# Kernel tuning notes

Measured on AMD Instinct MI355X. Metric: run time of the kernel, lower is better.

The kernel has to match this reference:

```python
import jax, jax.numpy as jnp
import numpy as np

N, E, B = 100000, 800000, 32
TEXT, H, R, L = 768, 128, 8, 2
D, P, RANK = 16, 16, 8
SCALING = 16.0 / RANK  # LoRA alpha / rank


def setup_inputs() -> dict:
    key = jax.random.key(0)
    k = jax.random.split(key, 24)
    g = lambda i, shape, s=0.02: jax.random.normal(k[i], shape, dtype=jnp.float32) * s
    z = lambda shape: jnp.zeros(shape, jnp.float32)
    prop = g(7, (P, H), 0.02).at[0].set(0.0)  # property_emb row 0 zeroed (torch init)
    return {
        "x_text": jax.random.normal(k[0], (N, TEXT), jnp.float32),
        "x_path": jax.random.normal(k[1], (N, TEXT), jnp.float32),
        "text_proj_w": g(2, (TEXT, H)), "text_proj_b": z((H,)),
        "path_proj_w": g(3, (TEXT, H)), "path_proj_b": z((H,)),
        "domain_emb": g(4, (D, H), 1.0),
        "property_emb": prop,
        "path_fusion_w": g(5, (H, H)), "path_fusion_b": z((H,)),
        "pgate1_w": g(6, (2 * H, H)), "pgate1_b": z((H,)),
        "pgate2_w": g(8, (H, H)), "pgate2_b": z((H,)),
        "sem_w": g(9, (H, H)), "sem_b": z((H,)),
        "str_w": g(10, (H, H)), "str_b": z((H,)),
        "gate1_w": g(11, (2 * H, H)), "gate1_b": z((H,)),
        "gate2_w": g(12, (H, H)), "gate2_b": z((H,)),
        "rgcn_rel_w": g(13, (L, R, H, H)),
        "rgcn_root_w": g(14, (L, H, H)),
        "rgcn_bias": z((L, H)),
        "lora_a": g(15, (L, H, RANK)),
        "lora_b": g(16, (L, RANK, H)),
        "edge_index": jax.random.randint(k[17], (2, E), 0, N),
        "edge_type": jax.random.randint(k[18], (E,), 0, R),
        "batch": jnp.sort(jax.random.randint(k[19], (N,), 0, B)),
        "domain_ids": jax.random.randint(k[20], (B,), 0, D),
        "edge_property_id": jax.random.randint(k[21], (E,), 0, P),
    }


def reference(x_text, x_path, text_proj_w, text_proj_b, path_proj_w, path_proj_b,
              domain_emb, property_emb, path_fusion_w, path_fusion_b,
              pgate1_w, pgate1_b, pgate2_w, pgate2_b,
              sem_w, sem_b, str_w, str_b, gate1_w, gate1_b, gate2_w, gate2_b,
              rgcn_rel_w, rgcn_root_w, rgcn_bias, lora_a, lora_b,
              edge_index, edge_type, batch, domain_ids, edge_property_id):
    n = x_text.shape[0]
    num_layers, num_rel = rgcn_rel_w.shape[0], rgcn_rel_w.shape[1]
    src, dst = edge_index[0], edge_index[1]

    # text/path projections modulated by per-graph domain embedding
    h = x_text @ text_proj_w + text_proj_b                     # [N, H]
    d_nodes = domain_emb[domain_ids][batch]                    # [N, H]
    h = h * d_nodes
    path_ctx = (x_path @ path_proj_w + path_proj_b) * d_nodes
    path_ctx = path_ctx @ path_fusion_w + path_fusion_b
    pg = jax.nn.sigmoid(
        jax.nn.relu(jnp.concatenate([h, path_ctx], -1) @ pgate1_w + pgate1_b)
        @ pgate2_w + pgate2_b)
    h = pg * h + (1.0 - pg) * path_ctx

    # edge-property scatter-mean keyed by edge source node
    prop_ids = jnp.clip(edge_property_id, 0, property_emb.shape[0] - 1)
    pe = property_emb[prop_ids]                                # [E, H]
    ones_e = jnp.ones(src.shape, h.dtype)
    deg = jnp.maximum(jax.ops.segment_sum(ones_e, src, num_segments=n), 1.0)
    prop_agg = jax.ops.segment_sum(pe, src, num_segments=n) / deg[:, None]
    h = h + prop_agg                                           # _apply_property_prompts

    # RGCN: per-(dst, relation) mean aggregation, counts precomputed once
    seg = dst * num_rel + edge_type                            # composite segment id
    cnt = jax.ops.segment_sum(ones_e, seg, num_segments=n * num_rel)
    cnt = jnp.maximum(cnt, 1.0).reshape(n, num_rel, 1)

    curr = h
    for l in range(num_layers):
        curr_in = curr + prop_agg                              # _edge_property_message add
        sums = jax.ops.segment_sum(curr_in[src], seg, num_segments=n * num_rel)
        agg = sums.reshape(n, num_rel, -1) / cnt               # [N, R, H]
        conv = (jnp.einsum('nrh,rhd->nd', agg, rgcn_rel_w[l])
                + curr_in @ rgcn_root_w[l] + rgcn_bias[l])
        lora = (curr_in @ lora_a[l]) @ lora_b[l] * SCALING
        curr = jax.nn.relu(conv + lora)

    # semantic/structural gated fusion
    sem = h @ sem_w + sem_b
    stru = curr @ str_w + str_b
    fg = jax.nn.sigmoid(
        jax.nn.relu(jnp.concatenate([sem, stru], -1) @ gate1_w + gate1_b)
        @ gate2_w + gate2_b)
    return fg * sem + (1.0 - fg) * stru
```

## Files before the change

### kernel.cpp

```cpp
#include <hip/hip_runtime.h>
#include <cstdint>
#include <cstddef>

#define HDIM 128
#define GBM 64
#define GBK 32

__device__ __forceinline__ float sigmoidf_(float x) {
  return 1.0f / (1.0f + __expf(-x));
}

__global__ __launch_bounds__(256) void gemm128_f32(
    const float* __restrict__ A, const float* __restrict__ Wg,
    const float* __restrict__ bias, float* __restrict__ C,
    int M, int K, int accumulate, int post,
    long long strideWz, long long strideCz)
{
  __shared__ float As[GBM][GBK + 1];
  __shared__ float Ws[GBK][HDIM + 4];
  const float* Wp = Wg + (long long)blockIdx.z * strideWz;
  float* Cp = C + (long long)blockIdx.z * strideCz;
  const int m0 = blockIdx.x * GBM;
  const int tid = threadIdx.x;
  const int tx = tid & 15;
  const int ty = tid >> 4;

  float acc[4][8];
#pragma unroll
  for (int i = 0; i < 4; ++i)
#pragma unroll
    for (int j = 0; j < 8; ++j) acc[i][j] = 0.f;

  const int lar = tid >> 2;
  const int lac = (tid & 3) * 8;
  const int lwk = tid >> 3;
  const int lwj = (tid & 7) * 16;

  for (int k0 = 0; k0 < K; k0 += GBK) {
    float4 v0 = make_float4(0.f, 0.f, 0.f, 0.f), v1 = v0;
    {
      int gr = m0 + lar;
      if (gr < M) {
        const float* src = A + (long long)gr * K + (k0 + lac);
        v0 = *(const float4*)(src);
        v1 = *(const float4*)(src + 4);
      }
    }
    const float* wsrc = Wp + (long long)(k0 + lwk) * HDIM + lwj;
    float4 w0 = *(const float4*)(wsrc);
    float4 w1 = *(const float4*)(wsrc + 4);
    float4 w2 = *(const float4*)(wsrc + 8);
    float4 w3 = *(const float4*)(wsrc + 12);

    As[lar][lac + 0] = v0.x; As[lar][lac + 1] = v0.y;
    As[lar][lac + 2] = v0.z; As[lar][lac + 3] = v0.w;
    As[lar][lac + 4] = v1.x; As[lar][lac + 5] = v1.y;
    As[lar][lac + 6] = v1.z; As[lar][lac + 7] = v1.w;
    {
      float* wd = &Ws[lwk][lwj];
      wd[0]  = w0.x; wd[1]  = w0.y; wd[2]  = w0.z; wd[3]  = w0.w;
      wd[4]  = w1.x; wd[5]  = w1.y; wd[6]  = w1.z; wd[7]  = w1.w;
      wd[8]  = w2.x; wd[9]  = w2.y; wd[10] = w2.z; wd[11] = w2.w;
      wd[12] = w3.x; wd[13] = w3.y; wd[14] = w3.z; wd[15] = w3.w;
    }
    __syncthreads();

#pragma unroll 8
    for (int kk = 0; kk < GBK; ++kk) {
      float a0 = As[ty * 4 + 0][kk];
      float a1 = As[ty * 4 + 1][kk];
      float a2 = As[ty * 4 + 2][kk];
      float a3 = As[ty * 4 + 3][kk];
      float4 wa = *(const float4*)&Ws[kk][tx * 8];
      float4 wb = *(const float4*)&Ws[kk][tx * 8 + 4];
      float w[8] = {wa.x, wa.y, wa.z, wa.w, wb.x, wb.y, wb.z, wb.w};
#pragma unroll
      for (int j = 0; j < 8; ++j) {
        acc[0][j] += a0 * w[j];
        acc[1][j] += a1 * w[j];
        acc[2][j] += a2 * w[j];
        acc[3][j] += a3 * w[j];
      }
    }
    __syncthreads();
  }

#pragma unroll
  for (int i = 0; i < 4; ++i) {
    int gr = m0 + ty * 4 + i;
    if (gr >= M) continue;
    float* crow = Cp + (long long)gr * HDIM + tx * 8;
    float v[8];
#pragma unroll
    for (int j = 0; j < 8; ++j) v[j] = acc[i][j];
    if (bias) {
#pragma unroll
      for (int j = 0; j < 8; ++j) v[j] += bias[tx * 8 + j];
    }
    if (accumulate) {
      float4 c0 = *(const float4*)crow;
      float4 c1 = *(const float4*)(crow + 4);
      v[0] += c0.x; v[1] += c0.y; v[2] += c0.z; v[3] += c0.w;
      v[4] += c1.x; v[5] += c1.y; v[6] += c1.z; v[7] += c1.w;
    }
    if (post == 1) {
#pragma unroll
      for (int j = 0; j < 8; ++j) v[j] = fmaxf(v[j], 0.f);
    }
    *(float4*)crow = make_float4(v[0], v[1], v[2], v[3]);
    *(float4*)(crow + 4) = make_float4(v[4], v[5], v[6], v[7]);
  }
}

__global__ __launch_bounds__(256) void k_dnode(
    float* __restrict__ h, float* __restrict__ pc,
    const int* __restrict__ batch, const int* __restrict__ dom_ids,
    const float* __restrict__ dom_emb, int ntot)
{
  int idx = blockIdx.x * 256 + threadIdx.x;
  if (idx >= ntot) return;
  int n = idx >> 7, j = idx & 127;
  float d = dom_emb[dom_ids[batch[n]] * HDIM + j];
  h[idx] *= d;
  pc[idx] *= d;
}

__global__ __launch_bounds__(256) void k_combine(
    float* __restrict__ h, const float* __restrict__ pc,
    const float* __restrict__ pglin, const float* __restrict__ pa, int ntot)
{
  int idx = blockIdx.x * 256 + threadIdx.x;
  if (idx >= ntot) return;
  float pg = sigmoidf_(pglin[idx]);
  h[idx] = pg * h[idx] + (1.f - pg) * pc[idx] + pa[idx];
}

__global__ __launch_bounds__(256) void k_add(
    const float* __restrict__ a, const float* __restrict__ b,
    float* __restrict__ c, int ntot)
{
  int idx = blockIdx.x * 256 + threadIdx.x;
  if (idx >= ntot) return;
  c[idx] = a[idx] + b[idx];
}

__global__ __launch_bounds__(256) void k_out(
    const float* __restrict__ fglin, const float* __restrict__ sem,
    const float* __restrict__ stru, float* __restrict__ out, int ntot)
{
  int idx = blockIdx.x * 256 + threadIdx.x;
  if (idx >= ntot) return;
  float fg = sigmoidf_(fglin[idx]);
  out[idx] = fg * sem[idx] + (1.f - fg) * stru[idx];
}

__global__ __launch_bounds__(256) void k_edgecount(
    const int* __restrict__ ei, const int* __restrict__ etype,
    const int* __restrict__ epid, int* __restrict__ cntp,
    int* __restrict__ cnt8, int E)
{
  int e = blockIdx.x * 256 + threadIdx.x;
  if (e >= E) return;
  int s = ei[e];
  int d = ei[E + e];
  int et = etype[e];
  int p = epid[e];
  p = p < 0 ? 0 : (p > 15 ? 15 : p);
  atomicAdd(&cntp[s * 16 + p], 1);
  atomicAdd(&cnt8[d * 8 + et], 1);
}

__global__ __launch_bounds__(256) void k_propagg(
    const int* __restrict__ cntp, const float* __restrict__ pemb,
    float* __restrict__ pa, int ntot)
{
  int idx = blockIdx.x * 256 + threadIdx.x;
  if (idx >= ntot) return;
  int n = idx >> 7, j = idx & 127;
  int deg = 0;
  float acc = 0.f;
#pragma unroll
  for (int p = 0; p < 16; ++p) {
    int c = cntp[n * 16 + p];
    deg += c;
    acc += (float)c * pemb[p * HDIM + j];
  }
  pa[idx] = acc / (float)(deg > 1 ? deg : 1);
}

__global__ __launch_bounds__(256) void k_invcnt(
    const int* __restrict__ cnt8, float* __restrict__ invc, int ntot)
{
  int idx = blockIdx.x * 256 + threadIdx.x;
  if (idx >= ntot) return;
  int c = cnt8[idx];
  invc[idx] = 1.f / (float)(c > 1 ? c : 1);
}

__global__ __launch_bounds__(256) void k_scatter(
    const int* __restrict__ ei, const int* __restrict__ etype,
    const float* __restrict__ invc, const float* __restrict__ Y,
    float* __restrict__ conv, int E, int NN, int r0, int rc)
{
  int t = blockIdx.x * 256 + threadIdx.x;
  int e = t >> 7;
  int j = t & 127;
  if (e >= E) return;
  int et = etype[e];
  if (et < r0 || et >= r0 + rc) return;
  int s = ei[e];
  int d = ei[E + e];
  float w = invc[d * 8 + et];
  float v = Y[((long long)(et - r0) * NN + s) * HDIM + j] * w;
  atomicAdd(&conv[(long long)d * HDIM + j], v);
}

__global__ __launch_bounds__(256) void k_lora_relu(
    const float* __restrict__ xin, const float* __restrict__ conv,
    const float* __restrict__ la, const float* __restrict__ lb,
    float* __restrict__ outc, int NN)
{
  __shared__ float xs[16][129];
  __shared__ float las[128 * 8];
  __shared__ float lbs[8 * 128];
  __shared__ float Tsh[16][9];
  int tid = threadIdx.x;
  int n0 = blockIdx.x * 16;

  for (int i = tid; i < 1024; i += 256) {
    las[i] = la[i];
    lbs[i] = lb[i];
  }
  for (int i = tid; i < 16 * 128; i += 256) {
    int nn = i >> 7, j = i & 127;
    int g = n0 + nn;
    xs[nn][j] = (g < NN) ? xin[(long long)g * HDIM + j] : 0.f;
  }
  __syncthreads();

  if (tid < 128) {
    int nn = tid >> 3, r = tid & 7;
    float s = 0.f;
#pragma unroll 16
    for (int k = 0; k < 128; ++k) s += xs[nn][k] * las[k * 8 + r];
    Tsh[nn][r] = s;
  }
  __syncthreads();

  int nn = tid >> 4;
  int j0 = (tid & 15) * 8;
  int g = n0 + nn;
  if (g < NN) {
    const float* cv = conv + (long long)g * HDIM + j0;
    float* op = outc + (long long)g * HDIM + j0;
    float o[8];
#pragma unroll
    for (int jj = 0; jj < 8; ++jj) {
      float s = 0.f;
#pragma unroll
      for (int r = 0; r < 8; ++r) s += Tsh[nn][r] * lbs[r * HDIM + j0 + jj];
      float v = cv[jj] + 2.0f * s;
      o[jj] = fmaxf(v, 0.f);
    }
    *(float4*)op = make_float4(o[0], o[1], o[2], o[3]);
    *(float4*)(op + 4) = make_float4(o[4], o[5], o[6], o[7]);
  }
}

extern "C" void kernel_launch(void* const* d_in, const int* in_sizes, int n_in,
                              void* d_out, int out_size, void* d_ws, size_t ws_size,
                              hipStream_t stream)
{
  const int N = 100000, E = 800000, TEXT = 768, H = 128, R = 8, L = 2;
  const int NTOT = N * H;

  const float* x_text  = (const float*)d_in[0];
  const float* x_path  = (const float*)d_in[1];
  const float* text_w  = (const float*)d_in[2];
  const float* text_b  = (const float*)d_in[3];
  const float* path_w  = (const float*)d_in[4];
  const float* path_b  = (const float*)d_in[5];
  const float* dom_emb = (const float*)d_in[6];
  const float* prop_emb= (const float*)d_in[7];
  const float* pf_w    = (const float*)d_in[8];
  const float* pf_b    = (const float*)d_in[9];
  const float* pg1_w   = (const float*)d_in[10];
  const float* pg1_b   = (const float*)d_in[11];
  const float* pg2_w   = (const float*)d_in[12];
  const float* pg2_b   = (const float*)d_in[13];
  const float* sem_w   = (const float*)d_in[14];
  const float* sem_b   = (const float*)d_in[15];
  const float* str_w   = (const float*)d_in[16];
  const float* str_b   = (const float*)d_in[17];
  const float* g1_w    = (const float*)d_in[18];
  const float* g1_b    = (const float*)d_in[19];
  const float* g2_w    = (const float*)d_in[20];
  const float* g2_b    = (const float*)d_in[21];
  const float* rel_w   = (const float*)d_in[22];
  const float* root_w  = (const float*)d_in[23];
  const float* rbias   = (const float*)d_in[24];
  const float* lora_a  = (const float*)d_in[25];
  const float* lora_b  = (const float*)d_in[26];
  const int*   ei      = (const int*)d_in[27];
  const int*   etype   = (const int*)d_in[28];
  const int*   batch   = (const int*)d_in[29];
  const int*   dom_ids = (const int*)d_in[30];
  const int*   epid    = (const int*)d_in[31];
  float* out = (float*)d_out;

  const size_t NB = (size_t)NTOT * sizeof(float);
  char* p = (char*)d_ws;
  auto alloc = [&](size_t bytes) -> void* {
    char* q = p;
    p += (bytes + 255) & ~(size_t)255;
    return (void*)q;
  };
  float* hbuf  = (float*)alloc(NB);
  float* pabuf = (float*)alloc(NB);
  float* curr  = (float*)alloc(NB);
  float* cin   = (float*)alloc(NB);
  float* conv  = (float*)alloc(NB);
  float* tmp   = (float*)alloc(NB);
  int*   cntp  = (int*)alloc((size_t)N * 16 * 4);
  int*   cnt8  = (int*)alloc((size_t)N * 8 * 4);
  float* invc  = (float*)alloc((size_t)N * 8 * 4);
  size_t used = (size_t)(p - (char*)d_ws);

  float* ybuf = tmp;
  int RC = 1;
  if (ws_size > used) {
    size_t k = (ws_size - used) / NB;
    if (k >= 1) {
      RC = (int)(k < 8 ? k : 8);
      ybuf = (float*)alloc(NB * (size_t)RC);
    }
  }

  const int GM = (N + GBM - 1) / GBM;
  const int EWG = (NTOT + 255) / 256;

  auto gemm = [&](const float* A, const float* W, const float* b, float* C,
                  int K, int accv, int post, int zc,
                  long long swz, long long scz) {
    gemm128_f32<<<dim3(GM, 1, zc), dim3(256), 0, stream>>>(
        A, W, b, C, N, K, accv, post, swz, scz);
  };

  hipMemsetAsync(cntp, 0, (size_t)N * 24 * 4, stream);
  k_edgecount<<<(E + 255) / 256, 256, 0, stream>>>(ei, etype, epid, cntp, cnt8, E);
  k_propagg<<<EWG, 256, 0, stream>>>(cntp, prop_emb, pabuf, NTOT);
  k_invcnt<<<(N * 8 + 255) / 256, 256, 0, stream>>>(cnt8, invc, N * 8);

  gemm(x_text, text_w, text_b, hbuf, TEXT, 0, 0, 1, 0, 0);
  gemm(x_path, path_w, path_b, curr, TEXT, 0, 0, 1, 0, 0);
  k_dnode<<<EWG, 256, 0, stream>>>(hbuf, curr, batch, dom_ids, dom_emb, NTOT);
  gemm(curr, pf_w, pf_b, cin, H, 0, 0, 1, 0, 0);
  gemm(hbuf, pg1_w, pg1_b, conv, H, 0, 0, 1, 0, 0);
  gemm(cin, pg1_w + H * H, nullptr, conv, H, 1, 1, 1, 0, 0);
  gemm(conv, pg2_w, pg2_b, tmp, H, 0, 0, 1, 0, 0);
  k_combine<<<EWG, 256, 0, stream>>>(hbuf, cin, tmp, pabuf, NTOT);

  for (int l = 0; l < L; ++l) {
    const float* src = (l == 0) ? hbuf : curr;
    k_add<<<EWG, 256, 0, stream>>>(src, pabuf, cin, NTOT);
    gemm(cin, root_w + (size_t)l * H * H, rbias + (size_t)l * H,
         conv, H, 0, 0, 1, 0, 0);
    for (int r0 = 0; r0 < R; r0 += RC) {
      int rc = (R - r0) < RC ? (R - r0) : RC;
      gemm(cin, rel_w + ((size_t)l * R + r0) * H * H, nullptr, ybuf,
           H, 0, 0, rc, (long long)H * H, (long long)NTOT);
      k_scatter<<<(E * 128 + 255) / 256, 256, 0, stream>>>(
          ei, etype, invc, ybuf, conv, E, N, r0, rc);
    }
    k_lora_relu<<<(N + 15) / 16, 256, 0, stream>>>(
        cin, conv, lora_a + (size_t)l * H * 8, lora_b + (size_t)l * 8 * H,
        curr, N);
  }

  gemm(hbuf, sem_w, sem_b, conv, H, 0, 0, 1, 0, 0);
  gemm(curr, str_w, str_b, cin, H, 0, 0, 1, 0, 0);
  gemm(conv, g1_w, g1_b, tmp, H, 0, 0, 1, 0, 0);
  gemm(cin, g1_w + H * H, nullptr, tmp, H, 1, 1, 1, 0, 0);
  gemm(tmp, g2_w, g2_b, pabuf, H, 0, 0, 1, 0, 0);
  k_out<<<EWG, 256, 0, stream>>>(pabuf, conv, cin, out, NTOT);
}
```

Before: 3.732 ms.

## Replace per-relation transform-and-scatter with CSR gather aggregation then one fused GEMM

Builds a per-(dst, relation) CSR index once, using a prefix scan over the edge counts and an atomic fill of source ids. Each RGCN layer now gathers and mean-aggregates neighbour features into an [N, R*H] buffer, then does one K=1024 GEMM against the stacked relation weights. This removes the eight per-relation GEMMs and the float atomic scatter over E×128 elements. The shared GEMM kernel is also retiled to 128-row blocks with an 8x8 per-thread micro-tile and a transposed A tile. The cost is a large aggregation buffer whose size no longer checks the available workspace.

```diff
diff --git a/kernel.cpp b/kernel.cpp
--- a/kernel.cpp
+++ b/kernel.cpp
@@ -3,112 +3,112 @@
 #include <cstddef>
 
 #define HDIM 128
-#define GBM 64
-#define GBK 32
+#define TM 128
+#define TK 32
+#define SCHUNK 1024
 
 __device__ __forceinline__ float sigmoidf_(float x) {
   return 1.0f / (1.0f + __expf(-x));
 }
 
-__global__ __launch_bounds__(256) void gemm128_f32(
-    const float* __restrict__ A, const float* __restrict__ Wg,
+__global__ __launch_bounds__(256) void gemm128(
+    const float* __restrict__ A, const float* __restrict__ W,
     const float* __restrict__ bias, float* __restrict__ C,
-    int M, int K, int accumulate, int post,
-    long long strideWz, long long strideCz)
-{
-  __shared__ float As[GBM][GBK + 1];
-  __shared__ float Ws[GBK][HDIM + 4];
-  const float* Wp = Wg + (long long)blockIdx.z * strideWz;
-  float* Cp = C + (long long)blockIdx.z * strideCz;
-  const int m0 = blockIdx.x * GBM;
+    int M, int K, int accumulate, int post)
+{
+  __shared__ float At[TK][TM + 4];
+  __shared__ float Ws[TK][HDIM + 4];
+  const int m0 = blockIdx.x * TM;
   const int tid = threadIdx.x;
   const int tx = tid & 15;
   const int ty = tid >> 4;
 
-  float acc[4][8];
-#pragma unroll
-  for (int i = 0; i < 4; ++i)
+  float acc[8][8];
+#pragma unroll
+  for (int i = 0; i < 8; ++i)
 #pragma unroll
     for (int j = 0; j < 8; ++j) acc[i][j] = 0.f;
 
-  const int lar = tid >> 2;
-  const int lac = (tid & 3) * 8;
-  const int lwk = tid >> 3;
-  const int lwj = (tid & 7) * 16;
-
-  for (int k0 = 0; k0 < K; k0 += GBK) {
-    float4 v0 = make_float4(0.f, 0.f, 0.f, 0.f), v1 = v0;
-    {
-      int gr = m0 + lar;
-      if (gr < M) {
-        const float* src = A + (long long)gr * K + (k0 + lac);
-        v0 = *(const float4*)(src);
-        v1 = *(const float4*)(src + 4);
+  const int arow = tid >> 3;
+  const int ac4  = (tid & 7) * 4;
+  const int wrow = tid >> 5;
+  const int wc4  = (tid & 31) * 4;
+
+  for (int k0 = 0; k0 < K; k0 += TK) {
+#pragma unroll
+    for (int q = 0; q < 4; ++q) {
+      int row = q * 32 + arow;
+      int gr = m0 + row;
+      float4 v = make_float4(0.f, 0.f, 0.f, 0.f);
+      if (gr < M) v = *(const float4*)(A + (long long)gr * K + k0 + ac4);
+      At[ac4 + 0][row] = v.x;
+      At[ac4 + 1][row] = v.y;
+      At[ac4 + 2][row] = v.z;
+      At[ac4 + 3][row] = v.w;
+    }
+#pragma unroll
+    for (int q = 0; q < 4; ++q) {
+      int row = q * 8 + wrow;
+      float4 v = *(const float4*)(W + (long long)(k0 + row) * HDIM + wc4);
+      *(float4*)&Ws[row][wc4] = v;
+    }
+    __syncthreads();
+
+#pragma unroll 8
+    for (int kk = 0; kk < TK; ++kk) {
+      float4 a0 = *(const float4*)&At[kk][ty * 4];
+      float4 a1 = *(const float4*)&At[kk][64 + ty * 4];
+      float4 w0 = *(const float4*)&Ws[kk][tx * 4];
+      float4 w1 = *(const float4*)&Ws[kk][64 + tx * 4];
+      float a[8] = {a0.x, a0.y, a0.z, a0.w, a1.x, a1.y, a1.z, a1.w};
+      float w[8] = {w0.x, w0.y, w0.z, w0.w, w1.x, w1.y, w1.z, w1.w};
+#pragma unroll
+      for (int i = 0; i < 8; ++i)
+#pragma unroll
+        for (int j = 0; j < 8; ++j)
+          acc[i][j] += a[i] * w[j];
+    }
+    __syncthreads();
+  }
+
+  float bv[8];
+  if (bias) {
+#pragma unroll
+    for (int j = 0; j < 4; ++j) {
+      bv[j]     = bias[tx * 4 + j];
+      bv[4 + j] = bias[64 + tx * 4 + j];
+    }
+  } else {
+#pragma unroll
+    for (int j = 0; j < 8; ++j) bv[j] = 0.f;
+  }
+#pragma unroll
+  for (int i = 0; i < 8; ++i) {
+    int row = (i < 4) ? (ty * 4 + i) : (64 + ty * 4 + i - 4);
+    int gr = m0 + row;
+    if (gr >= M) continue;
+    float* cp = C + (long long)gr * HDIM;
+    float v0[4], v1[4];
+#pragma unroll
+    for (int j = 0; j < 4; ++j) {
+      v0[j] = acc[i][j] + bv[j];
+      v1[j] = acc[i][4 + j] + bv[4 + j];
+    }
+    if (accumulate) {
+      float4 c0 = *(const float4*)(cp + tx * 4);
+      float4 c1 = *(const float4*)(cp + 64 + tx * 4);
+      v0[0] += c0.x; v0[1] += c0.y; v0[2] += c0.z; v0[3] += c0.w;
+      v1[0] += c1.x; v1[1] += c1.y; v1[2] += c1.z; v1[3] += c1.w;
+    }
+    if (post == 1) {
+#pragma unroll
+      for (int j = 0; j < 4; ++j) {
+        v0[j] = fmaxf(v0[j], 0.f);
+        v1[j] = fmaxf(v1[j], 0.f);
       }
     }
-    const float* wsrc = Wp + (long long)(k0 + lwk) * HDIM + lwj;
-    float4 w0 = *(const float4*)(wsrc);
-    float4 w1 = *(const float4*)(wsrc + 4);
-    float4 w2 = *(const float4*)(wsrc + 8);
-    float4 w3 = *(const float4*)(wsrc + 12);
-
-    As[lar][lac + 0] = v0.x; As[lar][lac + 1] = v0.y;
-    As[lar][lac + 2] = v0.z; As[lar][lac + 3] = v0.w;
-    As[lar][lac + 4] = v1.x; As[lar][lac + 5] = v1.y;
-    As[lar][lac + 6] = v1.z; As[lar][lac + 7] = v1.w;
-    {
-      float* wd = &Ws[lwk][lwj];
-      wd[0]  = w0.x; wd[1]  = w0.y; wd[2]  = w0.z; wd[3]  = w0.w;
-      wd[4]  = w1.x; wd[5]  = w1.y; wd[6]  = w1.z; wd[7]  = w1.w;
-      wd[8]  = w2.x; wd[9]  = w2.y; wd[10] = w2.z; wd[11] = w2.w;
-      wd[12] = w3.x; wd[13] = w3.y; wd[14] = w3.z; wd[15] = w3.w;
-    }
-    __syncthreads();
-
-#pragma unroll 8
-    for (int kk = 0; kk < GBK; ++kk) {
-      float a0 = As[ty * 4 + 0][kk];
-      float a1 = As[ty * 4 + 1][kk];
-      float a2 = As[ty * 4 + 2][kk];
-      float a3 = As[ty * 4 + 3][kk];
-      float4 wa = *(const float4*)&Ws[kk][tx * 8];
-      float4 wb = *(const float4*)&Ws[kk][tx * 8 + 4];
-      float w[8] = {wa.x, wa.y, wa.z, wa.w, wb.x, wb.y, wb.z, wb.w};
-#pragma unroll
-      for (int j = 0; j < 8; ++j) {
-        acc[0][j] += a0 * w[j];
-        acc[1][j] += a1 * w[j];
-        acc[2][j] += a2 * w[j];
-        acc[3][j] += a3 * w[j];
-      }
-    }
-    __syncthreads();
-  }
-
-#pragma unroll
-  for (int i = 0; i < 4; ++i) {
-    int gr = m0 + ty * 4 + i;
-    if (gr >= M) continue;
-    float* crow = Cp + (long long)gr * HDIM + tx * 8;
-    float v[8];
-#pragma unroll
-    for (int j = 0; j < 8; ++j) v[j] = acc[i][j];
-    if (bias) {
-#pragma unroll
-      for (int j = 0; j < 8; ++j) v[j] += bias[tx * 8 + j];
-    }
-    if (accumulate) {
-      float4 c0 = *(const float4*)crow;
-      float4 c1 = *(const float4*)(crow + 4);
-      v[0] += c0.x; v[1] += c0.y; v[2] += c0.z; v[3] += c0.w;
-      v[4] += c1.x; v[5] += c1.y; v[6] += c1.z; v[7] += c1.w;
-    }
-    if (post == 1) {
-#pragma unroll
-      for (int j = 0; j < 8; ++j) v[j] = fmaxf(v[j], 0.f);
-    }
-    *(float4*)crow = make_float4(v[0], v[1], v[2], v[3]);
-    *(float4*)(crow + 4) = make_float4(v[4], v[5], v[6], v[7]);
+    *(float4*)(cp + tx * 4)      = make_float4(v0[0], v0[1], v0[2], v0[3]);
+    *(float4*)(cp + 64 + tx * 4) = make_float4(v1[0], v1[1], v1[2], v1[3]);
   }
 }
 
@@ -188,31 +188,109 @@
   pa[idx] = acc / (float)(deg > 1 ? deg : 1);
 }
 
-__global__ __launch_bounds__(256) void k_invcnt(
-    const int* __restrict__ cnt8, float* __restrict__ invc, int ntot)
-{
-  int idx = blockIdx.x * 256 + threadIdx.x;
-  if (idx >= ntot) return;
-  int c = cnt8[idx];
-  invc[idx] = 1.f / (float)(c > 1 ? c : 1);
-}
-
-__global__ __launch_bounds__(256) void k_scatter(
+__global__ __launch_bounds__(256) void s_scan1(
+    const int* __restrict__ cnt, int* __restrict__ base,
+    int* __restrict__ bsum, int n)
+{
+  __shared__ int sa[256], sb[256];
+  const int tid = threadIdx.x;
+  const int i0 = blockIdx.x * SCHUNK + tid * 4;
+  int4 v = make_int4(0, 0, 0, 0);
+  if (i0 + 4 <= n) v = *(const int4*)(cnt + i0);
+  else {
+    if (i0 + 0 < n) v.x = cnt[i0];
+    if (i0 + 1 < n) v.y = cnt[i0 + 1];
+    if (i0 + 2 < n) v.z = cnt[i0 + 2];
+    if (i0 + 3 < n) v.w = cnt[i0 + 3];
+  }
+  int l0 = v.x, l1 = l0 + v.y, l2 = l1 + v.z, l3 = l2 + v.w;
+  sa[tid] = l3;
+  __syncthreads();
+  int* s = sa;
+  int* d = sb;
+  for (int off = 1; off < 256; off <<= 1) {
+    int x = s[tid];
+    if (tid >= off) x += s[tid - off];
+    d[tid] = x;
+    __syncthreads();
+    int* t = s; s = d; d = t;
+  }
+  int excl = s[tid] - l3;
+  if (i0 + 0 < n) base[i0]     = excl;
+  if (i0 + 1 < n) base[i0 + 1] = excl + l0;
+  if (i0 + 2 < n) base[i0 + 2] = excl + l1;
+  if (i0 + 3 < n) base[i0 + 3] = excl + l2;
+  if (tid == 255) bsum[blockIdx.x] = s[255];
+}
+
+__global__ __launch_bounds__(256) void s_scan2(int* __restrict__ bsum, int n)
+{
+  __shared__ int sa[256], sb[256];
+  const int tid = threadIdx.x;
+  const int i0 = tid * 4;
+  int v0 = 0, v1 = 0, v2 = 0, v3 = 0;
+  if (i0 + 0 < n) v0 = bsum[i0];
+  if (i0 + 1 < n) v1 = bsum[i0 + 1];
+  if (i0 + 2 < n) v2 = bsum[i0 + 2];
+  if (i0 + 3 < n) v3 = bsum[i0 + 3];
+  int l0 = v0, l1 = l0 + v1, l2 = l1 + v2, l3 = l2 + v3;
+  sa[tid] = l3;
+  __syncthreads();
+  int* s = sa;
+  int* d = sb;
+  for (int off = 1; off < 256; off <<= 1) {
+    int x = s[tid];
+    if (tid >= off) x += s[tid - off];
+    d[tid] = x;
+    __syncthreads();
+    int* t = s; s = d; d = t;
+  }
+  int excl = s[tid] - l3;
+  if (i0 + 0 < n) bsum[i0]     = excl;
+  if (i0 + 1 < n) bsum[i0 + 1] = excl + l0;
+  if (i0 + 2 < n) bsum[i0 + 2] = excl + l1;
+  if (i0 + 3 < n) bsum[i0 + 3] = excl + l2;
+}
+
+__global__ __launch_bounds__(256) void s_scan3(
+    int* __restrict__ base, const int* __restrict__ bsum, int n)
+{
+  int i = blockIdx.x * 256 + threadIdx.x;
+  if (i < n) base[i] += bsum[i >> 10];
+}
+
+__global__ __launch_bounds__(256) void k_fill(
     const int* __restrict__ ei, const int* __restrict__ etype,
-    const float* __restrict__ invc, const float* __restrict__ Y,
-    float* __restrict__ conv, int E, int NN, int r0, int rc)
-{
-  int t = blockIdx.x * 256 + threadIdx.x;
-  int e = t >> 7;
-  int j = t & 127;
+    int* __restrict__ base, int* __restrict__ srcs, int E)
+{
+  int e = blockIdx.x * 256 + threadIdx.x;
   if (e >= E) return;
-  int et = etype[e];
-  if (et < r0 || et >= r0 + rc) return;
   int s = ei[e];
   int d = ei[E + e];
-  float w = invc[d * 8 + et];
-  float v = Y[((long long)(et - r0) * NN + s) * HDIM + j] * w;
-  atomicAdd(&conv[(long long)d * HDIM + j], v);
+  int et = etype[e];
+  int pos = atomicAdd(&base[d * 8 + et], 1);
+  srcs[pos] = s;
+}
+
+__global__ __launch_bounds__(256) void k_aggregate(
+    const int* __restrict__ base, const int* __restrict__ cnt,
+    const int* __restrict__ srcs, const float* __restrict__ x,
+    float* __restrict__ agg, int ncell)
+{
+  int cell = (blockIdx.x * 256 + threadIdx.x) >> 6;
+  int lane = threadIdx.x & 63;
+  if (cell >= ncell) return;
+  int c = cnt[cell];
+  int end = base[cell];
+  float ax = 0.f, ay = 0.f;
+  for (int i = end - c; i < end; ++i) {
+    int s = srcs[i];
+    float2 v = *(const float2*)&x[(long long)s * HDIM + lane * 2];
+    ax += v.x;
+    ay += v.y;
+  }
+  float w = 1.f / (float)(c > 1 ? c : 1);
+  *(float2*)&agg[(long long)cell * HDIM + lane * 2] = make_float2(ax * w, ay * w);
 }
 
 __global__ __launch_bounds__(256) void k_lora_relu(
@@ -273,6 +351,8 @@
 {
   const int N = 100000, E = 800000, TEXT = 768, H = 128, R = 8, L = 2;
   const int NTOT = N * H;
+  const int NCELL = N * R;
+  const int NCH = (NCELL + SCHUNK - 1) / SCHUNK;
 
   const float* x_text  = (const float*)d_in[0];
   const float* x_path  = (const float*)d_in[1];
@@ -320,67 +400,54 @@
   float* curr  = (float*)alloc(NB);
   float* cin   = (float*)alloc(NB);
   float* conv  = (float*)alloc(NB);
-  float* tmp   = (float*)alloc(NB);
   int*   cntp  = (int*)alloc((size_t)N * 16 * 4);
   int*   cnt8  = (int*)alloc((size_t)N * 8 * 4);
-  float* invc  = (float*)alloc((size_t)N * 8 * 4);
-  size_t used = (size_t)(p - (char*)d_ws);
-
-  float* ybuf = tmp;
-  int RC = 1;
-  if (ws_size > used) {
-    size_t k = (ws_size - used) / NB;
-    if (k >= 1) {
-      RC = (int)(k < 8 ? k : 8);
-      ybuf = (float*)alloc(NB * (size_t)RC);
-    }
-  }
-
-  const int GM = (N + GBM - 1) / GBM;
+  int*   base  = (int*)alloc((size_t)NCELL * 4);
+  int*   srcs  = (int*)alloc((size_t)E * 4);
+  int*   bsum  = (int*)alloc((size_t)1024 * 4);
+  float* agg   = (float*)alloc((size_t)NCELL * H * sizeof(float));
+
+  const int GM = (N + TM - 1) / TM;
   const int EWG = (NTOT + 255) / 256;
 
   auto gemm = [&](const float* A, const float* W, const float* b, float* C,
-                  int K, int accv, int post, int zc,
-                  long long swz, long long scz) {
-    gemm128_f32<<<dim3(GM, 1, zc), dim3(256), 0, stream>>>(
-        A, W, b, C, N, K, accv, post, swz, scz);
+                  int K, int accv, int post) {
+    gemm128<<<dim3(GM), dim3(256), 0, stream>>>(A, W, b, C, N, K, accv, post);
   };
 
   hipMemsetAsync(cntp, 0, (size_t)N * 24 * 4, stream);
   k_edgecount<<<(E + 255) / 256, 256, 0, stream>>>(ei, etype, epid, cntp, cnt8, E);
   k_propagg<<<EWG, 256, 0, stream>>>(cntp, prop_emb, pabuf, NTOT);
-  k_invcnt<<<(N * 8 + 255) / 256, 256, 0, stream>>>(cnt8, invc, N * 8);
-
-  gemm(x_text, text_w, text_b, hbuf, TEXT, 0, 0, 1, 0, 0);
-  gemm(x_path, path_w, path_b, curr, TEXT, 0, 0, 1, 0, 0);
+  s_scan1<<<NCH, 256, 0, stream>>>(cnt8, base, bsum, NCELL);
+  s_scan2<<<1, 256, 0, stream>>>(bsum, NCH);
+  s_scan3<<<(NCELL + 255) / 256, 256, 0, stream>>>(base, bsum, NCELL);
+  k_fill<<<(E + 255) / 256, 256, 0, stream>>>(ei, etype, base, srcs, E);
+
+  gemm(x_text, text_w, text_b, hbuf, TEXT, 0, 0);
+  gemm(x_path, path_w, path_b, curr, TEXT, 0, 0);
   k_dnode<<<EWG, 256, 0, stream>>>(hbuf, curr, batch, dom_ids, dom_emb, NTOT);
-  gemm(curr, pf_w, pf_b, cin, H, 0, 0, 1, 0, 0);
-  gemm(hbuf, pg1_w, pg1_b, conv, H, 0, 0, 1, 0, 0);
-  gemm(cin, pg1_w + H * H, nullptr, conv, H, 1, 1, 1, 0, 0);
-  gemm(conv, pg2_w, pg2_b, tmp, H, 0, 0, 1, 0, 0);
-  k_combine<<<EWG, 256, 0, stream>>>(hbuf, cin, tmp, pabuf, NTOT);
+  gemm(curr, pf_w, pf_b, cin, H, 0, 0);
+  gemm(hbuf, pg1_w, pg1_b, conv, H, 0, 0);
+  gemm(cin, pg1_w + H * H, nullptr, conv, H, 1, 1);
+  gemm(conv, pg2_w, pg2_b, curr, H, 0, 0);
+  k_combine<<<EWG, 256, 0, stream>>>(hbuf, cin, curr, pabuf, NTOT);
 
   for (int l = 0; l < L; ++l) {
     const float* src = (l == 0) ? hbuf : curr;
     k_add<<<EWG, 256, 0, stream>>>(src, pabuf, cin, NTOT);
-    gemm(cin, root_w + (size_t)l * H * H, rbias + (size_t)l * H,
-         conv, H, 0, 0, 1, 0, 0);
-    for (int r0 = 0; r0 < R; r0 += RC) {
-      int rc = (R - r0) < RC ? (R - r0) : RC;
-      gemm(cin, rel_w + ((size_t)l * R + r0) * H * H, nullptr, ybuf,
-           H, 0, 0, rc, (long long)H * H, (long long)NTOT);
-      k_scatter<<<(E * 128 + 255) / 256, 256, 0, stream>>>(
-          ei, etype, invc, ybuf, conv, E, N, r0, rc);
-    }
+    k_aggregate<<<NCELL / 4, 256, 0, stream>>>(base, cnt8, srcs, cin, agg, NCELL);
+    gemm(agg, rel_w + (size_t)l * R * H * H, rbias + (size_t)l * H,
+         conv, R * H, 0, 0);
+    gemm(cin, root_w + (size_t)l * H * H, nullptr, conv, H, 1, 0);
     k_lora_relu<<<(N + 15) / 16, 256, 0, stream>>>(
         cin, conv, lora_a + (size_t)l * H * 8, lora_b + (size_t)l * 8 * H,
         curr, N);
   }
 
-  gemm(hbuf, sem_w, sem_b, conv, H, 0, 0, 1, 0, 0);
-  gemm(curr, str_w, str_b, cin, H, 0, 0, 1, 0, 0);
-  gemm(conv, g1_w, g1_b, tmp, H, 0, 0, 1, 0, 0);
-  gemm(cin, g1_w + H * H, nullptr, tmp, H, 1, 1, 1, 0, 0);
-  gemm(tmp, g2_w, g2_b, pabuf, H, 0, 0, 1, 0, 0);
-  k_out<<<EWG, 256, 0, stream>>>(pabuf, conv, cin, out, NTOT);
-}
+  gemm(hbuf, sem_w, sem_b, conv, H, 0, 0);
+  gemm(curr, str_w, str_b, cin, H, 0, 0);
+  gemm(conv, g1_w, g1_b, pabuf, H, 0, 0);
+  gemm(cin, g1_w + H * H, nullptr, pabuf, H, 1, 1);
+  gemm(pabuf, g2_w, g2_b, hbuf, H, 0, 0);
+  k_out<<<EWG, 256, 0, stream>>>(hbuf, conv, cin, out, NTOT);
+}
```

New measurement: 3.401 ms. -8.9%, faster.
